# Performance work log

Hardware: AMD Instinct MI355X
Metric: run time of the kernel (lower is better)

## Reference

```python
import jax, jax.numpy as jnp
import numpy as np

EPS = 1e-5  # nn.LayerNorm default eps


def setup_inputs() -> dict:
    key = jax.random.key(0)
    k1, k2, k3 = jax.random.split(key, 3)
    B, S, V, D = 16, 2048, 32, 128
    x = jax.random.normal(k1, (B, S, V), dtype=jnp.float32)
    # per-variable Linear(1, D): weight [D,1] -> flattened to [V, D]
    W = jax.random.normal(k2, (V, D), dtype=jnp.float32)
    b = jax.random.normal(k3, (V, D), dtype=jnp.float32) * 0.1
    gamma = jnp.ones((V, D), dtype=jnp.float32)
    beta = jnp.zeros((V, D), dtype=jnp.float32)
    return {"x": x, "W": W, "b": b, "gamma": gamma, "beta": beta}


def reference(x, W, b, gamma, beta):
    # x: [B,S,V]; W,b,gamma,beta: [V,D]
    # Fused equivalent of per-variable Linear(1,D) -> LayerNorm(D) -> ReLU,
    # stacked on a new variable axis: output [B,S,V,D].
    h = x[..., None] * W + b                      # [B,S,V,D]
    mu = jnp.mean(h, axis=-1, keepdims=True)
    var = jnp.mean(jnp.square(h - mu), axis=-1, keepdims=True)
    normed = (h - mu) * jax.lax.rsqrt(var + EPS)
    out = jax.nn.relu(normed * gamma + beta)
    return out
```

## Files before the change

### kernel.cpp

```cpp
#include <hip/hip_runtime.h>


#define EPS 1e-5f

constexpr int D = 128;
constexpr int V = 32;

__global__ __launch_bounds__(64) void precompute_kernel(
    const float* __restrict__ W,
    const float* __restrict__ Bv,
    const float* __restrict__ G,
    float* __restrict__ A,
    float* __restrict__ C,
    float* __restrict__ coef) {
  const int v = blockIdx.x;
  const int t = threadIdx.x;
  const float w0 = W[v * D + t],  w1 = W[v * D + t + 64];
  const float b0 = Bv[v * D + t], b1 = Bv[v * D + t + 64];

  float sw = w0 + w1, sb = b0 + b1;
  #pragma unroll
  for (int off = 32; off > 0; off >>= 1) {
    sw += __shfl_down(sw, off);
    sb += __shfl_down(sb, off);
  }
  const float mW = __shfl(sw, 0) * (1.0f / D);
  const float mB = __shfl(sb, 0) * (1.0f / D);

  const float cw0 = w0 - mW, cw1 = w1 - mW;
  const float cb0 = b0 - mB, cb1 = b1 - mB;

  float sww = cw0 * cw0 + cw1 * cw1;
  float swb = cw0 * cb0 + cw1 * cb1;
  float sbb = cb0 * cb0 + cb1 * cb1;
  #pragma unroll
  for (int off = 32; off > 0; off >>= 1) {
    sww += __shfl_down(sww, off);
    swb += __shfl_down(swb, off);
    sbb += __shfl_down(sbb, off);
  }
  if (t == 0) {
    coef[v * 4 + 0] = sww * (1.0f / D);
    coef[v * 4 + 1] = 2.0f * swb * (1.0f / D);
    coef[v * 4 + 2] = sbb * (1.0f / D) + EPS;
  }

  const float g0 = G[v * D + t], g1 = G[v * D + t + 64];
  A[v * D + t]      = cw0 * g0;
  A[v * D + t + 64] = cw1 * g1;
  C[v * D + t]      = cb0 * g0;
  C[v * D + t + 64] = cb1 * g1;
}

__global__ __launch_bounds__(256) void fused_kernel(
    const float* __restrict__ x,
    const float* __restrict__ A,
    const float* __restrict__ C,
    const float* __restrict__ beta,
    const float* __restrict__ coef,
    float* __restrict__ out,
    int n4) {
  const int stride = gridDim.x * blockDim.x;
  for (int i = blockIdx.x * blockDim.x + threadIdx.x; i < n4; i += stride) {
    const int d4  = i & 31;
    const int row = i >> 5;
    const int v   = row & (V - 1);

    const float xv = x[row];

    const int pidx = (v << 5) + d4;
    const float4 a4  = reinterpret_cast<const float4*>(A)[pidx];
    const float4 c4  = reinterpret_cast<const float4*>(C)[pidx];
    const float4 be4 = reinterpret_cast<const float4*>(beta)[pidx];

    const float p2 = coef[v * 4 + 0];
    const float p1 = coef[v * 4 + 1];
    const float p0 = coef[v * 4 + 2];
    const float r  = rsqrtf(fmaf(xv, fmaf(xv, p2, p1), p0));

    float4 o;
    o.x = fmaxf(fmaf(fmaf(xv, a4.x, c4.x), r, be4.x), 0.0f);
    o.y = fmaxf(fmaf(fmaf(xv, a4.y, c4.y), r, be4.y), 0.0f);
    o.z = fmaxf(fmaf(fmaf(xv, a4.z, c4.z), r, be4.z), 0.0f);
    o.w = fmaxf(fmaf(fmaf(xv, a4.w, c4.w), r, be4.w), 0.0f);

    reinterpret_cast<float4*>(out)[i] = o;
  }
}

extern "C" void kernel_launch(void* const* d_in, const int* in_sizes, int n_in,
                              void* d_out, int out_size, void* d_ws, size_t ws_size,
                              hipStream_t stream) {
  const float* x     = (const float*)d_in[0];
  const float* W     = (const float*)d_in[1];
  const float* b     = (const float*)d_in[2];
  const float* gamma = (const float*)d_in[3];
  const float* beta  = (const float*)d_in[4];
  float* out = (float*)d_out;

  float* A    = (float*)d_ws;
  float* C    = A + V * D;
  float* coef = C + V * D;

  precompute_kernel<<<V, 64, 0, stream>>>(W, b, gamma, A, C, coef);

  const int n4 = out_size / 4;
  const int threads = 256;
  const int blocks = 16384;
  fused_kernel<<<blocks, threads, 0, stream>>>(x, A, C, beta, coef, out, n4);
}
```

Baseline: 583.2 us.

## Fuse parameter precompute into main kernel with register-resident per-variable coefficients

Removes the separate precompute kernel launch. Each block now recomputes the per-variable centered weight, bias and variance coefficients in registers for its 8 variables, then loops over a chunk of rows with those values held fixed. This avoids per-element reloads of A/C/beta/coef and the grid-stride index math. Output writes use nontemporal stores to reduce cache pollution on the large output. The trade-off is that the small precompute is repeated in every block.

After: 520.6 us. 1.12x faster.

```diff
diff --git a/kernel.cpp b/kernel.cpp
--- a/kernel.cpp
+++ b/kernel.cpp
@@ -5,86 +5,77 @@
 
 constexpr int D = 128;
 constexpr int V = 32;
+constexpr int BS_TOTAL = 16 * 2048;
+constexpr int NB = 512;
+constexpr int CHUNK = BS_TOTAL / NB;
 
-__global__ __launch_bounds__(64) void precompute_kernel(
+typedef float vfloat4 __attribute__((ext_vector_type(4)));
+
+__global__ __launch_bounds__(256) void fused_kernel(
+    const float* __restrict__ x,
     const float* __restrict__ W,
     const float* __restrict__ Bv,
     const float* __restrict__ G,
-    float* __restrict__ A,
-    float* __restrict__ C,
-    float* __restrict__ coef) {
-  const int v = blockIdx.x;
+    const float* __restrict__ Beta,
+    float* __restrict__ out) {
   const int t = threadIdx.x;
-  const float w0 = W[v * D + t],  w1 = W[v * D + t + 64];
-  const float b0 = Bv[v * D + t], b1 = Bv[v * D + t + 64];
+  const int d4 = t & 31;
+  const int vl = t >> 5;
+  const int group = blockIdx.x & 3;
+  const int blk = blockIdx.x >> 2;
+  const int v = group * 8 + vl;
 
-  float sw = w0 + w1, sb = b0 + b1;
+  const int pidx = v * (D / 4) + d4;
+  const vfloat4 w4  = reinterpret_cast<const vfloat4*>(W)[pidx];
+  const vfloat4 b4  = reinterpret_cast<const vfloat4*>(Bv)[pidx];
+  const vfloat4 g4  = reinterpret_cast<const vfloat4*>(G)[pidx];
+  const vfloat4 be4 = reinterpret_cast<const vfloat4*>(Beta)[pidx];
+
+  float sw = w4.x + w4.y + w4.z + w4.w;
+  float sb = b4.x + b4.y + b4.z + b4.w;
   #pragma unroll
-  for (int off = 32; off > 0; off >>= 1) {
-    sw += __shfl_down(sw, off);
-    sb += __shfl_down(sb, off);
+  for (int off = 16; off > 0; off >>= 1) {
+    sw += __shfl_xor(sw, off);
+    sb += __shfl_xor(sb, off);
   }
-  const float mW = __shfl(sw, 0) * (1.0f / D);
-  const float mB = __shfl(sb, 0) * (1.0f / D);
+  const float mW = sw * (1.0f / D);
+  const float mB = sb * (1.0f / D);
 
-  const float cw0 = w0 - mW, cw1 = w1 - mW;
-  const float cb0 = b0 - mB, cb1 = b1 - mB;
+  vfloat4 a4 = w4 - mW;
+  vfloat4 c4 = b4 - mB;
 
-  float sww = cw0 * cw0 + cw1 * cw1;
-  float swb = cw0 * cb0 + cw1 * cb1;
-  float sbb = cb0 * cb0 + cb1 * cb1;
+  float sww = a4.x * a4.x + a4.y * a4.y + a4.z * a4.z + a4.w * a4.w;
+  float swb = a4.x * c4.x + a4.y * c4.y + a4.z * c4.z + a4.w * c4.w;
+  float sbb = c4.x * c4.x + c4.y * c4.y + c4.z * c4.z + c4.w * c4.w;
   #pragma unroll
-  for (int off = 32; off > 0; off >>= 1) {
-    sww += __shfl_down(sww, off);
-    swb += __shfl_down(swb, off);
-    sbb += __shfl_down(sbb, off);
+  for (int off = 16; off > 0; off >>= 1) {
+    sww += __shfl_xor(sww, off);
+    swb += __shfl_xor(swb, off);
+    sbb += __shfl_xor(sbb, off);
   }
-  if (t == 0) {
-    coef[v * 4 + 0] = sww * (1.0f / D);
-    coef[v * 4 + 1] = 2.0f * swb * (1.0f / D);
-    coef[v * 4 + 2] = sbb * (1.0f / D) + EPS;
-  }
+  const float p2 = sww * (1.0f / D);
+  const float p1 = 2.0f * swb * (1.0f / D);
+  const float p0 = sbb * (1.0f / D) + EPS;
 
-  const float g0 = G[v * D + t], g1 = G[v * D + t + 64];
-  A[v * D + t]      = cw0 * g0;
-  A[v * D + t + 64] = cw1 * g1;
-  C[v * D + t]      = cb0 * g0;
-  C[v * D + t + 64] = cb1 * g1;
-}
+  a4 *= g4;
+  c4 *= g4;
 
-__global__ __launch_bounds__(256) void fused_kernel(
-    const float* __restrict__ x,
-    const float* __restrict__ A,
-    const float* __restrict__ C,
-    const float* __restrict__ beta,
-    const float* __restrict__ coef,
-    float* __restrict__ out,
-    int n4) {
-  const int stride = gridDim.x * blockDim.x;
-  for (int i = blockIdx.x * blockDim.x + threadIdx.x; i < n4; i += stride) {
-    const int d4  = i & 31;
-    const int row = i >> 5;
-    const int v   = row & (V - 1);
+  const int bs0 = blk * CHUNK;
+  vfloat4* op = reinterpret_cast<vfloat4*>(out);
 
+  #pragma unroll 4
+  for (int i = 0; i < CHUNK; ++i) {
+    const int row = (bs0 + i) * V + v;
     const float xv = x[row];
+    const float r = rsqrtf(fmaf(xv, fmaf(xv, p2, p1), p0));
 
-    const int pidx = (v << 5) + d4;
-    const float4 a4  = reinterpret_cast<const float4*>(A)[pidx];
-    const float4 c4  = reinterpret_cast<const float4*>(C)[pidx];
-    const float4 be4 = reinterpret_cast<const float4*>(beta)[pidx];
-
-    const float p2 = coef[v * 4 + 0];
-    const float p1 = coef[v * 4 + 1];
-    const float p0 = coef[v * 4 + 2];
-    const float r  = rsqrtf(fmaf(xv, fmaf(xv, p2, p1), p0));
-
-    float4 o;
+    vfloat4 o;
     o.x = fmaxf(fmaf(fmaf(xv, a4.x, c4.x), r, be4.x), 0.0f);
     o.y = fmaxf(fmaf(fmaf(xv, a4.y, c4.y), r, be4.y), 0.0f);
     o.z = fmaxf(fmaf(fmaf(xv, a4.z, c4.z), r, be4.z), 0.0f);
     o.w = fmaxf(fmaf(fmaf(xv, a4.w, c4.w), r, be4.w), 0.0f);
 
-    reinterpret_cast<float4*>(out)[i] = o;
+    __builtin_nontemporal_store(o, op + row * (D / 4) + d4);
   }
 }
 
@@ -98,14 +89,5 @@
   const float* beta  = (const float*)d_in[4];
   float* out = (float*)d_out;
 
-  float* A    = (float*)d_ws;
-  float* C    = A + V * D;
-  float* coef = C + V * D;
-
-  precompute_kernel<<<V, 64, 0, stream>>>(W, b, gamma, A, C, coef);
-
-  const int n4 = out_size / 4;
-  const int threads = 256;
-  const int blocks = 16384;
-  fused_kernel<<<blocks, threads, 0, stream>>>(x, A, C, beta, coef, out, n4);
+  fused_kernel<<<4 * NB, 256, 0, stream>>>(x, W, b, gamma, beta, out);
 }
```
